# Kernel tuning notes

Measured on AMD Instinct MI355X. Metric: run time of the kernel, lower is better.

The kernel has to match this reference:

```python
import jax, jax.numpy as jnp
import numpy as np
from jax import lax


def setup_inputs() -> dict:
    key = jax.random.key(0)
    ks = jax.random.split(key, 10)
    T, S, B, L, H = 256, 1024, 1, 2, 1024
    sc = 1.0 / np.sqrt(H)  # torch LSTM/Linear init scale
    return {
        "input_sequence": jax.random.normal(ks[0], (T, B, H), jnp.float32),
        "encoder_out": jax.random.normal(ks[1], (S, B, H), jnp.float32),
        "hidden_state": jax.random.normal(ks[2], (L, B, H), jnp.float32),
        "cell_state": jax.random.normal(ks[3], (L, B, H), jnp.float32),
        "w_ih": jax.random.uniform(ks[4], (L, 4 * H, H), jnp.float32, -sc, sc),
        "w_hh": jax.random.uniform(ks[5], (L, 4 * H, H), jnp.float32, -sc, sc),
        "b_ih": jax.random.uniform(ks[6], (L, 4 * H), jnp.float32, -sc, sc),
        "b_hh": jax.random.uniform(ks[7], (L, 4 * H), jnp.float32, -sc, sc),
        "w_concat": jax.random.uniform(ks[8], (H, 2 * H), jnp.float32, -sc, sc),
        "b_concat": jax.random.uniform(ks[9], (H,), jnp.float32, -sc, sc),
    }


def reference(input_sequence, encoder_out, hidden_state, cell_state,
              w_ih, w_hh, b_ih, b_hh, w_concat, b_concat):
    T = input_sequence.shape[0]
    L = w_ih.shape[0]

    def step(carry, _):
        h, c, x = carry  # h,c: [L,1,H]; x: [1,H]
        hs, cs = [], []
        inp = x
        for l in range(L):  # stacked LSTM layers (small, static)
            gates = inp @ w_ih[l].T + h[l] @ w_hh[l].T + b_ih[l] + b_hh[l]  # [1,4H]
            i, f, g, o = jnp.split(gates, 4, axis=-1)  # torch gate order i,f,g,o
            c_new = jax.nn.sigmoid(f) * c[l] + jax.nn.sigmoid(i) * jnp.tanh(g)
            h_new = jax.nn.sigmoid(o) * jnp.tanh(c_new)
            hs.append(h_new)
            cs.append(c_new)
            inp = h_new
        h = jnp.stack(hs)  # [L,1,H]
        c = jnp.stack(cs)
        # Luong 'dot' attention: scores [S,1,1] = encoder_out @ h_last^T (B=1)
        scores = jnp.einsum('sbh,bh->sb', encoder_out, h[-1])[..., None]
        w = jax.nn.softmax(scores, axis=0)               # softmax over source dim
        context = jnp.sum(encoder_out * w, axis=0)        # [1,H]
        cat = jnp.concatenate([context, h[-1]], axis=-1)  # [1,2H]
        attn_h = jnp.tanh(cat @ w_concat.T + b_concat)    # [1,H]
        return (h, c, attn_h), attn_h

    init = (hidden_state, cell_state, hidden_state[-1])
    _, outputs = lax.scan(step, init, None, length=T)
    return outputs  # [T,1,H]
```

## Files before the change

kernel.cpp:

```cpp
#include <hip/hip_runtime.h>
#include <cstdint>
#include <cstddef>


#define TSTEPS 256
#define HDIM   1024
#define NBLK   256
#define NTHR   256

#define WS_X    0
#define WS_H0   1024
#define WS_H1   3072
#define WS_C0   5120
#define WS_C1   6144
#define WS_SC   7168
#define WS_Y2   8192
#define WS_MT   16384
#define SLOTS_OFF_BYTES ((size_t)(WS_MT + 1024 * 1024) * sizeof(float))
#define SLOT_STRIDE 16

__device__ __forceinline__ float wred_sum(float v) {
#pragma unroll
  for (int m = 32; m >= 1; m >>= 1) v += __shfl_xor(v, m, 64);
  return v;
}
__device__ __forceinline__ float wred_max(float v) {
#pragma unroll
  for (int m = 32; m >= 1; m >>= 1) v = fmaxf(v, __shfl_xor(v, m, 64));
  return v;
}

__device__ __forceinline__ float2 aload2(const float* p) {
  unsigned long long u = __hip_atomic_load((unsigned long long*)(uintptr_t)p,
                                           __ATOMIC_RELAXED, __HIP_MEMORY_SCOPE_AGENT);
  float2 r;
  r.x = __uint_as_float((unsigned)u);
  r.y = __uint_as_float((unsigned)(u >> 32));
  return r;
}
__device__ __forceinline__ void astoref(float* p, float v) {
  __hip_atomic_store((unsigned*)p, __float_as_uint(v), __ATOMIC_RELAXED,
                     __HIP_MEMORY_SCOPE_AGENT);
}

__device__ __forceinline__ void gbar(int* slots, int gen) {
  __syncthreads();
  if (threadIdx.x == 0)
    __hip_atomic_store(&slots[blockIdx.x * SLOT_STRIDE], gen, __ATOMIC_RELAXED,
                       __HIP_MEMORY_SCOPE_AGENT);
  int ok;
  do {
    int v = __hip_atomic_load(&slots[threadIdx.x * SLOT_STRIDE], __ATOMIC_RELAXED,
                              __HIP_MEMORY_SCOPE_AGENT);
    ok = (v >= gen);
    if (!ok) __builtin_amdgcn_s_sleep(2);
  } while (!__syncthreads_and(ok));
}

__device__ __forceinline__ float sigmoidf_(float x) { return 1.f / (1.f + __expf(-x)); }

__device__ __forceinline__ void load16_plain(const float* base, int l, float* r) {
#pragma unroll
  for (int i = 0; i < 8; ++i) {
    float2 a = *(const float2*)(base + 2 * l + 128 * i);
    r[2 * i] = a.x; r[2 * i + 1] = a.y;
  }
}
__device__ __forceinline__ void load16_agent(const float* base, int l, float* r) {
#pragma unroll
  for (int i = 0; i < 8; ++i) {
    float2 a = aload2(base + 2 * l + 128 * i);
    r[2 * i] = a.x; r[2 * i + 1] = a.y;
  }
}
__device__ __forceinline__ float dotrow(const float* row, int l, const float* x) {
  float p = 0.f;
#pragma unroll
  for (int i = 0; i < 8; ++i) {
    float2 wv = *(const float2*)(row + 2 * l + 128 * i);
    p += wv.x * x[2 * i] + wv.y * x[2 * i + 1];
  }
  return p;
}

__device__ __forceinline__ void lstm_cell(
    int k, int l, const float* __restrict__ wih, const float* __restrict__ whh,
    const float* __restrict__ bih, const float* __restrict__ bhh,
    const float* xr, const float* hr, const float* cold_src, float* cdst,
    float* hdst) {
  float gs[4];
#pragma unroll
  for (int g = 0; g < 4; ++g) {
    const float* wi = wih + (size_t)(g * HDIM + k) * HDIM;
    const float* wh = whh + (size_t)(g * HDIM + k) * HDIM;
    float p = dotrow(wi, l, xr) + dotrow(wh, l, hr);
    gs[g] = wred_sum(p);
  }
  if (l == 0) {
    float ig = sigmoidf_(gs[0] + bih[k] + bhh[k]);
    float fg = sigmoidf_(gs[1] + bih[HDIM + k] + bhh[HDIM + k]);
    float gg = tanhf(gs[2] + bih[2 * HDIM + k] + bhh[2 * HDIM + k]);
    float og = sigmoidf_(gs[3] + bih[3 * HDIM + k] + bhh[3 * HDIM + k]);
    float cn = fg * cold_src[k] + ig * gg;
    cdst[k] = cn;
    astoref(hdst + k, og * tanhf(cn));
  }
}

__global__ void __launch_bounds__(NTHR) decoder_persist(
    const float* __restrict__ enc,
    const float* __restrict__ hid,
    const float* __restrict__ cell,
    const float* __restrict__ w_ih,
    const float* __restrict__ w_hh,
    const float* __restrict__ b_ih,
    const float* __restrict__ b_hh,
    const float* __restrict__ wcat,
    const float* __restrict__ bcat,
    float* __restrict__ out,
    float* __restrict__ ws) {
  const int b = blockIdx.x;
  const int tid = threadIdx.x;
  const int w = tid >> 6;
  const int l = tid & 63;
  int* slots = (int*)((char*)ws + SLOTS_OFF_BYTES);
  float* MT = ws + WS_MT;

  {
    const int j0 = b << 2;
    const float* wr0 = wcat + (size_t)(j0 + 0) * 2048;
    const float* wr1 = wcat + (size_t)(j0 + 1) * 2048;
    const float* wr2 = wcat + (size_t)(j0 + 2) * 2048;
    const float* wr3 = wcat + (size_t)(j0 + 3) * 2048;
#pragma unroll
    for (int ii = 0; ii < 4; ++ii) {
      int s = (w << 8) + (ii << 6) + l;
      const float* er = enc + (size_t)s * HDIM;
      float a0 = 0.f, a1 = 0.f, a2 = 0.f, a3 = 0.f;
      for (int hh = 0; hh < HDIM; hh += 4) {
        float4 ev = *(const float4*)(er + hh);
        float4 w0 = *(const float4*)(wr0 + hh);
        float4 w1 = *(const float4*)(wr1 + hh);
        float4 w2 = *(const float4*)(wr2 + hh);
        float4 w3 = *(const float4*)(wr3 + hh);
        a0 += ev.x * w0.x + ev.y * w0.y + ev.z * w0.z + ev.w * w0.w;
        a1 += ev.x * w1.x + ev.y * w1.y + ev.z * w1.z + ev.w * w1.w;
        a2 += ev.x * w2.x + ev.y * w2.y + ev.z * w2.z + ev.w * w2.w;
        a3 += ev.x * w3.x + ev.y * w3.y + ev.z * w3.z + ev.w * w3.w;
      }
      MT[(size_t)(j0 + 0) * HDIM + s] = a0;
      MT[(size_t)(j0 + 1) * HDIM + s] = a1;
      MT[(size_t)(j0 + 2) * HDIM + s] = a2;
      MT[(size_t)(j0 + 3) * HDIM + s] = a3;
    }
  }
  __syncthreads();

  const float* wih1 = w_ih + (size_t)4096 * 1024;
  const float* whh1 = w_hh + (size_t)4096 * 1024;
  const float* bih1 = b_ih + 4096;
  const float* bhh1 = b_hh + 4096;

  for (int t = 0; t < TSTEPS; ++t) {
    const int par = t & 1;
    float* h0r = ws + WS_H0 + par * 1024;
    float* h0w = ws + WS_H0 + (par ^ 1) * 1024;
    float* h1r = ws + WS_H1 + par * 1024;
    float* h1w = ws + WS_H1 + (par ^ 1) * 1024;

    {
      const int k = (b << 2) + w;
      float xr[16], hr[16];
      if (t == 0) {
        load16_plain(hid + HDIM, l, xr);
        load16_plain(hid, l, hr);
      } else {
        load16_agent(ws + WS_X, l, xr);
        load16_agent(h0r, l, hr);
      }
      const float* csrc = (t == 0) ? cell : (ws + WS_C0);
      lstm_cell(k, l, w_ih, w_hh, b_ih, b_hh, xr, hr, csrc, ws + WS_C0, h0w);
    }
    gbar(slots, t * 4 + 1);

    {
      const int k = (b << 2) + w;
      float xr[16], hr[16];
      load16_agent(h0w, l, xr);
      if (t == 0) load16_plain(hid + HDIM, l, hr);
      else        load16_agent(h1r, l, hr);
      const float* csrc = (t == 0) ? (cell + HDIM) : (ws + WS_C1);
      lstm_cell(k, l, wih1, whh1, bih1, bhh1, xr, hr, csrc, ws + WS_C1, h1w);
    }
    gbar(slots, t * 4 + 2);

    {
      float hv[16];
      load16_agent(h1w, l, hv);
#pragma unroll
      for (int rr = 0; rr < 2; ++rr) {
        int r = (b << 2) + ((w & 1) << 1) + rr;
        const float* row = (w < 2) ? (enc + (size_t)r * HDIM)
                                   : (wcat + (size_t)r * 2048 + HDIM);
        float p = dotrow(row, l, hv);
        p = wred_sum(p);
        if (l == 0) {
          if (w < 2) astoref(ws + WS_SC + r, p);
          else       ws[WS_Y2 + r] = p;
        }
      }
    }
    gbar(slots, t * 4 + 3);

    {
      const int j = (b << 2) + w;
      float sc[16];
      load16_agent(ws + WS_SC, l, sc);
      float m = sc[0];
#pragma unroll
      for (int i = 1; i < 16; ++i) m = fmaxf(m, sc[i]);
      m = wred_max(m);
      float e[16];
      float d = 0.f;
#pragma unroll
      for (int i = 0; i < 16; ++i) { e[i] = __expf(sc[i] - m); d += e[i]; }
      d = wred_sum(d);
      const float* mrow = MT + (size_t)j * HDIM;
      float p = 0.f;
#pragma unroll
      for (int i = 0; i < 8; ++i) {
        float2 mv = *(const float2*)(mrow + 2 * l + 128 * i);
        p += mv.x * e[2 * i] + mv.y * e[2 * i + 1];
      }
      p = wred_sum(p);
      if (l == 0) {
        float a = tanhf(p / d + ws[WS_Y2 + j] + bcat[j]);
        astoref(ws + WS_X + j, a);
        out[(size_t)t * HDIM + j] = a;
      }
    }
    gbar(slots, t * 4 + 4);
  }
}

extern "C" void kernel_launch(void* const* d_in, const int* in_sizes, int n_in,
                              void* d_out, int out_size, void* d_ws, size_t ws_size,
                              hipStream_t stream) {
  const float* enc  = (const float*)d_in[1];
  const float* hid  = (const float*)d_in[2];
  const float* cel  = (const float*)d_in[3];
  const float* wih  = (const float*)d_in[4];
  const float* whh  = (const float*)d_in[5];
  const float* bih  = (const float*)d_in[6];
  const float* bhh  = (const float*)d_in[7];
  const float* wcat = (const float*)d_in[8];
  const float* bcat = (const float*)d_in[9];
  float* out = (float*)d_out;
  float* ws  = (float*)d_ws;

  hipLaunchKernelGGL(decoder_persist, dim3(NBLK), dim3(NTHR), 0, stream,
                     enc, hid, cel, wih, whh, bih, bhh, wcat, bcat, out, ws);
}
```

Baseline: 4.104 ms.

## Widen blocks to 1024 threads and stage shared vectors in LDS

Raises threads per block from 256 to 1024, with each wave now computing one gate row per hidden unit, or a half row or chunk in the later phases, instead of four gate rows per wave. The shared x/h vectors are loaded once per block into LDS rather than per wave through atomic float2 loads. Partial sums are combined through shared memory, and the softmax is spread across all 1024 threads. This shortens the serial per-wave work between grid barriers, at the cost of extra __syncthreads and a heavier barrier with more threads per block. It also caches the w_concat rows in LDS for the precompute.

```diff
diff --git a/kernel.cpp b/kernel.cpp
--- a/kernel.cpp
+++ b/kernel.cpp
@@ -6,7 +6,7 @@
 #define TSTEPS 256
 #define HDIM   1024
 #define NBLK   256
-#define NTHR   256
+#define NTHR   1024
 
 #define WS_X    0
 #define WS_H0   1024
@@ -14,7 +14,6 @@
 #define WS_C0   5120
 #define WS_C1   6144
 #define WS_SC   7168
-#define WS_Y2   8192
 #define WS_MT   16384
 #define SLOTS_OFF_BYTES ((size_t)(WS_MT + 1024 * 1024) * sizeof(float))
 #define SLOT_STRIDE 16
@@ -30,13 +29,10 @@
   return v;
 }
 
-__device__ __forceinline__ float2 aload2(const float* p) {
-  unsigned long long u = __hip_atomic_load((unsigned long long*)(uintptr_t)p,
-                                           __ATOMIC_RELAXED, __HIP_MEMORY_SCOPE_AGENT);
-  float2 r;
-  r.x = __uint_as_float((unsigned)u);
-  r.y = __uint_as_float((unsigned)(u >> 32));
-  return r;
+__device__ __forceinline__ float aloadf(const float* p) {
+  unsigned u = __hip_atomic_load((const unsigned*)(uintptr_t)p,
+                                 __ATOMIC_RELAXED, __HIP_MEMORY_SCOPE_AGENT);
+  return __uint_as_float(u);
 }
 __device__ __forceinline__ void astoref(float* p, float v) {
   __hip_atomic_store((unsigned*)p, __float_as_uint(v), __ATOMIC_RELAXED,
@@ -48,66 +44,20 @@
   if (threadIdx.x == 0)
     __hip_atomic_store(&slots[blockIdx.x * SLOT_STRIDE], gen, __ATOMIC_RELAXED,
                        __HIP_MEMORY_SCOPE_AGENT);
-  int ok;
+  int ok = 1;
   do {
-    int v = __hip_atomic_load(&slots[threadIdx.x * SLOT_STRIDE], __ATOMIC_RELAXED,
-                              __HIP_MEMORY_SCOPE_AGENT);
-    ok = (v >= gen);
-    if (!ok) __builtin_amdgcn_s_sleep(2);
+    if (threadIdx.x < NBLK) {
+      int v = __hip_atomic_load(&slots[threadIdx.x * SLOT_STRIDE],
+                                __ATOMIC_RELAXED, __HIP_MEMORY_SCOPE_AGENT);
+      ok = (v >= gen);
+      if (!ok) __builtin_amdgcn_s_sleep(2);
+    }
   } while (!__syncthreads_and(ok));
 }
 
 __device__ __forceinline__ float sigmoidf_(float x) { return 1.f / (1.f + __expf(-x)); }
 
-__device__ __forceinline__ void load16_plain(const float* base, int l, float* r) {
-#pragma unroll
-  for (int i = 0; i < 8; ++i) {
-    float2 a = *(const float2*)(base + 2 * l + 128 * i);
-    r[2 * i] = a.x; r[2 * i + 1] = a.y;
-  }
-}
-__device__ __forceinline__ void load16_agent(const float* base, int l, float* r) {
-#pragma unroll
-  for (int i = 0; i < 8; ++i) {
-    float2 a = aload2(base + 2 * l + 128 * i);
-    r[2 * i] = a.x; r[2 * i + 1] = a.y;
-  }
-}
-__device__ __forceinline__ float dotrow(const float* row, int l, const float* x) {
-  float p = 0.f;
-#pragma unroll
-  for (int i = 0; i < 8; ++i) {
-    float2 wv = *(const float2*)(row + 2 * l + 128 * i);
-    p += wv.x * x[2 * i] + wv.y * x[2 * i + 1];
-  }
-  return p;
-}
-
-__device__ __forceinline__ void lstm_cell(
-    int k, int l, const float* __restrict__ wih, const float* __restrict__ whh,
-    const float* __restrict__ bih, const float* __restrict__ bhh,
-    const float* xr, const float* hr, const float* cold_src, float* cdst,
-    float* hdst) {
-  float gs[4];
-#pragma unroll
-  for (int g = 0; g < 4; ++g) {
-    const float* wi = wih + (size_t)(g * HDIM + k) * HDIM;
-    const float* wh = whh + (size_t)(g * HDIM + k) * HDIM;
-    float p = dotrow(wi, l, xr) + dotrow(wh, l, hr);
-    gs[g] = wred_sum(p);
-  }
-  if (l == 0) {
-    float ig = sigmoidf_(gs[0] + bih[k] + bhh[k]);
-    float fg = sigmoidf_(gs[1] + bih[HDIM + k] + bhh[HDIM + k]);
-    float gg = tanhf(gs[2] + bih[2 * HDIM + k] + bhh[2 * HDIM + k]);
-    float og = sigmoidf_(gs[3] + bih[3 * HDIM + k] + bhh[3 * HDIM + k]);
-    float cn = fg * cold_src[k] + ig * gg;
-    cdst[k] = cn;
-    astoref(hdst + k, og * tanhf(cn));
-  }
-}
-
-__global__ void __launch_bounds__(NTHR) decoder_persist(
+__global__ void __launch_bounds__(NTHR, 4) decoder_persist(
     const float* __restrict__ enc,
     const float* __restrict__ hid,
     const float* __restrict__ cell,
@@ -125,34 +75,41 @@
   const int l = tid & 63;
   int* slots = (int*)((char*)ws + SLOTS_OFF_BYTES);
   float* MT = ws + WS_MT;
+  const int j0 = b << 2;
+
+  __shared__ float sh_x[HDIM];
+  __shared__ float sh_h[HDIM];
+  __shared__ __align__(16) float sh_es[HDIM];
+  __shared__ __align__(16) float sh_wc[4][HDIM];
+  __shared__ float sh_g[16];
+  __shared__ float sh_r[16];
+  __shared__ float sh_p[16];
+  __shared__ float sh_q[16];
+  __shared__ float sh_y2[4];
 
   {
-    const int j0 = b << 2;
-    const float* wr0 = wcat + (size_t)(j0 + 0) * 2048;
-    const float* wr1 = wcat + (size_t)(j0 + 1) * 2048;
-    const float* wr2 = wcat + (size_t)(j0 + 2) * 2048;
-    const float* wr3 = wcat + (size_t)(j0 + 3) * 2048;
-#pragma unroll
-    for (int ii = 0; ii < 4; ++ii) {
-      int s = (w << 8) + (ii << 6) + l;
-      const float* er = enc + (size_t)s * HDIM;
-      float a0 = 0.f, a1 = 0.f, a2 = 0.f, a3 = 0.f;
-      for (int hh = 0; hh < HDIM; hh += 4) {
-        float4 ev = *(const float4*)(er + hh);
-        float4 w0 = *(const float4*)(wr0 + hh);
-        float4 w1 = *(const float4*)(wr1 + hh);
-        float4 w2 = *(const float4*)(wr2 + hh);
-        float4 w3 = *(const float4*)(wr3 + hh);
-        a0 += ev.x * w0.x + ev.y * w0.y + ev.z * w0.z + ev.w * w0.w;
-        a1 += ev.x * w1.x + ev.y * w1.y + ev.z * w1.z + ev.w * w1.w;
-        a2 += ev.x * w2.x + ev.y * w2.y + ev.z * w2.z + ev.w * w2.w;
-        a3 += ev.x * w3.x + ev.y * w3.y + ev.z * w3.z + ev.w * w3.w;
-      }
-      MT[(size_t)(j0 + 0) * HDIM + s] = a0;
-      MT[(size_t)(j0 + 1) * HDIM + s] = a1;
-      MT[(size_t)(j0 + 2) * HDIM + s] = a2;
-      MT[(size_t)(j0 + 3) * HDIM + s] = a3;
-    }
+#pragma unroll
+    for (int rep = 0; rep < 4; ++rep)
+      sh_wc[rep][tid & 1023] = wcat[(size_t)(j0 + rep) * 2048 + tid];
+    __syncthreads();
+    const int s = (w << 6) + l;
+    const float* er = enc + (size_t)s * HDIM;
+    float a0 = 0.f, a1 = 0.f, a2 = 0.f, a3 = 0.f;
+    for (int hh = 0; hh < HDIM; hh += 4) {
+      float4 ev = *(const float4*)(er + hh);
+      float4 w0 = *(const float4*)&sh_wc[0][hh];
+      float4 w1 = *(const float4*)&sh_wc[1][hh];
+      float4 w2 = *(const float4*)&sh_wc[2][hh];
+      float4 w3 = *(const float4*)&sh_wc[3][hh];
+      a0 += ev.x * w0.x + ev.y * w0.y + ev.z * w0.z + ev.w * w0.w;
+      a1 += ev.x * w1.x + ev.y * w1.y + ev.z * w1.z + ev.w * w1.w;
+      a2 += ev.x * w2.x + ev.y * w2.y + ev.z * w2.z + ev.w * w2.w;
+      a3 += ev.x * w3.x + ev.y * w3.y + ev.z * w3.z + ev.w * w3.w;
+    }
+    MT[(size_t)(j0 + 0) * HDIM + s] = a0;
+    MT[(size_t)(j0 + 1) * HDIM + s] = a1;
+    MT[(size_t)(j0 + 2) * HDIM + s] = a2;
+    MT[(size_t)(j0 + 3) * HDIM + s] = a3;
   }
   __syncthreads();
 
@@ -169,74 +126,137 @@
     float* h1w = ws + WS_H1 + (par ^ 1) * 1024;
 
     {
-      const int k = (b << 2) + w;
-      float xr[16], hr[16];
       if (t == 0) {
-        load16_plain(hid + HDIM, l, xr);
-        load16_plain(hid, l, hr);
+        sh_x[tid] = hid[HDIM + tid];
+        sh_h[tid] = hid[tid];
       } else {
-        load16_agent(ws + WS_X, l, xr);
-        load16_agent(h0r, l, hr);
-      }
-      const float* csrc = (t == 0) ? cell : (ws + WS_C0);
-      lstm_cell(k, l, w_ih, w_hh, b_ih, b_hh, xr, hr, csrc, ws + WS_C0, h0w);
+        sh_x[tid] = aloadf(ws + WS_X + tid);
+        sh_h[tid] = aloadf(h0r + tid);
+      }
+      __syncthreads();
+      const int d = w >> 2, g = w & 3, k = j0 + d;
+      const float* wi = w_ih + (size_t)((g << 10) + k) * HDIM;
+      const float* wh = w_hh + (size_t)((g << 10) + k) * HDIM;
+      float p = 0.f;
+#pragma unroll
+      for (int i = 0; i < 8; ++i) {
+        float2 wv = *(const float2*)(wi + 2 * l + 128 * i);
+        float2 hv = *(const float2*)(wh + 2 * l + 128 * i);
+        float2 xv = *(const float2*)(sh_x + 2 * l + 128 * i);
+        float2 rv = *(const float2*)(sh_h + 2 * l + 128 * i);
+        p += wv.x * xv.x + wv.y * xv.y + hv.x * rv.x + hv.y * rv.y;
+      }
+      p = wred_sum(p);
+      if (l == 0) sh_g[w] = p;
+      __syncthreads();
+      if (tid < 4) {
+        const int k2 = j0 + tid;
+        float ig = sigmoidf_(sh_g[(tid << 2) + 0] + b_ih[k2] + b_hh[k2]);
+        float fg = sigmoidf_(sh_g[(tid << 2) + 1] + b_ih[HDIM + k2] + b_hh[HDIM + k2]);
+        float gg = tanhf   (sh_g[(tid << 2) + 2] + b_ih[2 * HDIM + k2] + b_hh[2 * HDIM + k2]);
+        float og = sigmoidf_(sh_g[(tid << 2) + 3] + b_ih[3 * HDIM + k2] + b_hh[3 * HDIM + k2]);
+        float cold = (t == 0) ? cell[k2] : ws[WS_C0 + k2];
+        float cn = fg * cold + ig * gg;
+        ws[WS_C0 + k2] = cn;
+        astoref(h0w + k2, og * tanhf(cn));
+      }
     }
     gbar(slots, t * 4 + 1);
 
     {
-      const int k = (b << 2) + w;
-      float xr[16], hr[16];
-      load16_agent(h0w, l, xr);
-      if (t == 0) load16_plain(hid + HDIM, l, hr);
-      else        load16_agent(h1r, l, hr);
-      const float* csrc = (t == 0) ? (cell + HDIM) : (ws + WS_C1);
-      lstm_cell(k, l, wih1, whh1, bih1, bhh1, xr, hr, csrc, ws + WS_C1, h1w);
+      sh_x[tid] = aloadf(h0w + tid);
+      if (t == 0) sh_h[tid] = hid[HDIM + tid];
+      else        sh_h[tid] = aloadf(h1r + tid);
+      __syncthreads();
+      const int d = w >> 2, g = w & 3, k = j0 + d;
+      const float* wi = wih1 + (size_t)((g << 10) + k) * HDIM;
+      const float* wh = whh1 + (size_t)((g << 10) + k) * HDIM;
+      float p = 0.f;
+#pragma unroll
+      for (int i = 0; i < 8; ++i) {
+        float2 wv = *(const float2*)(wi + 2 * l + 128 * i);
+        float2 hv = *(const float2*)(wh + 2 * l + 128 * i);
+        float2 xv = *(const float2*)(sh_x + 2 * l + 128 * i);
+        float2 rv = *(const float2*)(sh_h + 2 * l + 128 * i);
+        p += wv.x * xv.x + wv.y * xv.y + hv.x * rv.x + hv.y * rv.y;
+      }
+      p = wred_sum(p);
+      if (l == 0) sh_g[w] = p;
+      __syncthreads();
+      if (tid < 4) {
+        const int k2 = j0 + tid;
+        float ig = sigmoidf_(sh_g[(tid << 2) + 0] + bih1[k2] + bhh1[k2]);
+        float fg = sigmoidf_(sh_g[(tid << 2) + 1] + bih1[HDIM + k2] + bhh1[HDIM + k2]);
+        float gg = tanhf   (sh_g[(tid << 2) + 2] + bih1[2 * HDIM + k2] + bhh1[2 * HDIM + k2]);
+        float og = sigmoidf_(sh_g[(tid << 2) + 3] + bih1[3 * HDIM + k2] + bhh1[3 * HDIM + k2]);
+        float cold = (t == 0) ? cell[HDIM + k2] : ws[WS_C1 + k2];
+        float cn = fg * cold + ig * gg;
+        ws[WS_C1 + k2] = cn;
+        astoref(h1w + k2, og * tanhf(cn));
+      }
     }
     gbar(slots, t * 4 + 2);
 
     {
-      float hv[16];
-      load16_agent(h1w, l, hv);
-#pragma unroll
-      for (int rr = 0; rr < 2; ++rr) {
-        int r = (b << 2) + ((w & 1) << 1) + rr;
-        const float* row = (w < 2) ? (enc + (size_t)r * HDIM)
-                                   : (wcat + (size_t)r * 2048 + HDIM);
-        float p = dotrow(row, l, hv);
-        p = wred_sum(p);
-        if (l == 0) {
-          if (w < 2) astoref(ws + WS_SC + r, p);
-          else       ws[WS_Y2 + r] = p;
+      sh_x[tid] = aloadf(h1w + tid);
+      __syncthreads();
+      const int rw = w & 7;
+      const int d = rw >> 1, half = rw & 1;
+      const float* row = (w < 8)
+          ? (enc  + (size_t)(j0 + d) * 1024 + half * 512)
+          : (wcat + (size_t)(j0 + d) * 2048 + 1024 + half * 512);
+      float p = 0.f;
+#pragma unroll
+      for (int i = 0; i < 4; ++i) {
+        float2 wv = *(const float2*)(row + 2 * l + 128 * i);
+        float2 xv = *(const float2*)(sh_x + half * 512 + 2 * l + 128 * i);
+        p += wv.x * xv.x + wv.y * xv.y;
+      }
+      p = wred_sum(p);
+      if (l == 0) sh_g[w] = p;
+      __syncthreads();
+      if (tid < 8) {
+        if (tid < 4) {
+          float sc = sh_g[2 * tid] + sh_g[2 * tid + 1];
+          astoref(ws + WS_SC + j0 + tid, sc);
+        } else {
+          int d2 = tid - 4;
+          sh_y2[d2] = sh_g[8 + 2 * d2] + sh_g[9 + 2 * d2];
         }
       }
     }
     gbar(slots, t * 4 + 3);
 
     {
-      const int j = (b << 2) + w;
-      float sc[16];
-      load16_agent(ws + WS_SC, l, sc);
-      float m = sc[0];
-#pragma unroll
-      for (int i = 1; i < 16; ++i) m = fmaxf(m, sc[i]);
-      m = wred_max(m);
-      float e[16];
-      float d = 0.f;
-#pragma unroll
-      for (int i = 0; i < 16; ++i) { e[i] = __expf(sc[i] - m); d += e[i]; }
-      d = wred_sum(d);
-      const float* mrow = MT + (size_t)j * HDIM;
-      float p = 0.f;
-#pragma unroll
-      for (int i = 0; i < 8; ++i) {
-        float2 mv = *(const float2*)(mrow + 2 * l + 128 * i);
-        p += mv.x * e[2 * i] + mv.y * e[2 * i + 1];
-      }
-      p = wred_sum(p);
-      if (l == 0) {
-        float a = tanhf(p / d + ws[WS_Y2 + j] + bcat[j]);
-        astoref(ws + WS_X + j, a);
-        out[(size_t)t * HDIM + j] = a;
+      float sc = aloadf(ws + WS_SC + tid);
+      float m = wred_max(sc);
+      if (l == 0) sh_r[w] = m;
+      __syncthreads();
+      float bm = sh_r[0];
+#pragma unroll
+      for (int i = 1; i < 16; ++i) bm = fmaxf(bm, sh_r[i]);
+      float e = __expf(sc - bm);
+      sh_es[tid] = e;
+      float ps = wred_sum(e);
+      if (l == 0) sh_p[w] = ps;
+      __syncthreads();
+      const int d = w & 3, chunk = w >> 2, k = j0 + d;
+      const float* mrow = MT + (size_t)k * HDIM + (chunk << 8);
+      float4 mv = *(const float4*)(mrow + 4 * l);
+      float4 ev = *(const float4*)(&sh_es[(chunk << 8) + 4 * l]);
+      float p = mv.x * ev.x + mv.y * ev.y + mv.z * ev.z + mv.w * ev.w;
+      p = wred_sum(p);
+      if (l == 0) sh_q[w] = p;
+      __syncthreads();
+      if (tid < 4) {
+        const int k2 = j0 + tid;
+        float denom = 0.f;
+#pragma unroll
+        for (int i = 0; i < 16; ++i) denom += sh_p[i];
+        float numer = sh_q[tid] + sh_q[4 + tid] + sh_q[8 + tid] + sh_q[12 + tid];
+        float a = tanhf(numer / denom + sh_y2[tid] + bcat[k2]);
+        astoref(ws + WS_X + k2, a);
+        out[(size_t)t * HDIM + k2] = a;
       }
     }
     gbar(slots, t * 4 + 4);
```

Measured after the change: 4.685 ms. +14.2%, slower.

## Replace grid barriers with tagged dataflow slots and register-resident weights

Applied to the files above, without the earlier changes.

Removes the four grid-wide barriers per timestep. Producers now write 64-bit values that carry a generation tag, and consumer waves poll for them per element, then stage the data into LDS under workgroup-scope flags. Block size doubles to 512 threads so each block's LSTM weight rows, attention rows and the precomputed M rows stay in registers for the whole run instead of being reloaded every step. Correctness depends on the tags matching, and spin-waiting inside LDS could deadlock if waves are not scheduled fairly. Register pressure is much higher.

```diff
diff --git a/kernel.cpp b/kernel.cpp
--- a/kernel.cpp
+++ b/kernel.cpp
@@ -6,18 +6,15 @@
 #define TSTEPS 256
 #define HDIM   1024
 #define NBLK   256
-#define NTHR   256
-
-#define WS_X    0
-#define WS_H0   1024
-#define WS_H1   3072
-#define WS_C0   5120
-#define WS_C1   6144
-#define WS_SC   7168
-#define WS_Y2   8192
-#define WS_MT   16384
-#define SLOTS_OFF_BYTES ((size_t)(WS_MT + 1024 * 1024) * sizeof(float))
-#define SLOT_STRIDE 16
+#define NTHR   512
+
+typedef unsigned long long u64;
+
+#define WX   0
+#define WH0  1024
+#define WH1  3072
+#define WSC  5120
+#define WMT  6144
 
 __device__ __forceinline__ float wred_sum(float v) {
 #pragma unroll
@@ -29,85 +26,48 @@
   for (int m = 32; m >= 1; m >>= 1) v = fmaxf(v, __shfl_xor(v, m, 64));
   return v;
 }
-
-__device__ __forceinline__ float2 aload2(const float* p) {
-  unsigned long long u = __hip_atomic_load((unsigned long long*)(uintptr_t)p,
-                                           __ATOMIC_RELAXED, __HIP_MEMORY_SCOPE_AGENT);
-  float2 r;
-  r.x = __uint_as_float((unsigned)u);
-  r.y = __uint_as_float((unsigned)(u >> 32));
-  return r;
-}
-__device__ __forceinline__ void astoref(float* p, float v) {
-  __hip_atomic_store((unsigned*)p, __float_as_uint(v), __ATOMIC_RELAXED,
-                     __HIP_MEMORY_SCOPE_AGENT);
-}
-
-__device__ __forceinline__ void gbar(int* slots, int gen) {
-  __syncthreads();
-  if (threadIdx.x == 0)
-    __hip_atomic_store(&slots[blockIdx.x * SLOT_STRIDE], gen, __ATOMIC_RELAXED,
-                       __HIP_MEMORY_SCOPE_AGENT);
-  int ok;
-  do {
-    int v = __hip_atomic_load(&slots[threadIdx.x * SLOT_STRIDE], __ATOMIC_RELAXED,
-                              __HIP_MEMORY_SCOPE_AGENT);
-    ok = (v >= gen);
-    if (!ok) __builtin_amdgcn_s_sleep(2);
-  } while (!__syncthreads_and(ok));
-}
-
-__device__ __forceinline__ float sigmoidf_(float x) { return 1.f / (1.f + __expf(-x)); }
-
-__device__ __forceinline__ void load16_plain(const float* base, int l, float* r) {
-#pragma unroll
-  for (int i = 0; i < 8; ++i) {
-    float2 a = *(const float2*)(base + 2 * l + 128 * i);
-    r[2 * i] = a.x; r[2 * i + 1] = a.y;
-  }
-}
-__device__ __forceinline__ void load16_agent(const float* base, int l, float* r) {
-#pragma unroll
-  for (int i = 0; i < 8; ++i) {
-    float2 a = aload2(base + 2 * l + 128 * i);
-    r[2 * i] = a.x; r[2 * i + 1] = a.y;
-  }
-}
-__device__ __forceinline__ float dotrow(const float* row, int l, const float* x) {
-  float p = 0.f;
-#pragma unroll
-  for (int i = 0; i < 8; ++i) {
-    float2 wv = *(const float2*)(row + 2 * l + 128 * i);
-    p += wv.x * x[2 * i] + wv.y * x[2 * i + 1];
-  }
-  return p;
-}
-
-__device__ __forceinline__ void lstm_cell(
-    int k, int l, const float* __restrict__ wih, const float* __restrict__ whh,
-    const float* __restrict__ bih, const float* __restrict__ bhh,
-    const float* xr, const float* hr, const float* cold_src, float* cdst,
-    float* hdst) {
-  float gs[4];
-#pragma unroll
-  for (int g = 0; g < 4; ++g) {
-    const float* wi = wih + (size_t)(g * HDIM + k) * HDIM;
-    const float* wh = whh + (size_t)(g * HDIM + k) * HDIM;
-    float p = dotrow(wi, l, xr) + dotrow(wh, l, hr);
-    gs[g] = wred_sum(p);
-  }
-  if (l == 0) {
-    float ig = sigmoidf_(gs[0] + bih[k] + bhh[k]);
-    float fg = sigmoidf_(gs[1] + bih[HDIM + k] + bhh[HDIM + k]);
-    float gg = tanhf(gs[2] + bih[2 * HDIM + k] + bhh[2 * HDIM + k]);
-    float og = sigmoidf_(gs[3] + bih[3 * HDIM + k] + bhh[3 * HDIM + k]);
-    float cn = fg * cold_src[k] + ig * gg;
-    cdst[k] = cn;
-    astoref(hdst + k, og * tanhf(cn));
-  }
-}
-
-__global__ void __launch_bounds__(NTHR) decoder_persist(
+__device__ __forceinline__ void astore64(u64* p, int tag, float v) {
+  u64 x = ((u64)(unsigned)tag << 32) | (u64)(unsigned)__float_as_uint(v);
+  __hip_atomic_store(p, x, __ATOMIC_RELAXED, __HIP_MEMORY_SCOPE_AGENT);
+}
+__device__ __forceinline__ u64 aload64(const u64* p) {
+  return __hip_atomic_load(p, __ATOMIC_RELAXED, __HIP_MEMORY_SCOPE_AGENT);
+}
+__device__ __forceinline__ void lds_set(int* f, int v) {
+  __hip_atomic_store(f, v, __ATOMIC_RELEASE, __HIP_MEMORY_SCOPE_WORKGROUP);
+}
+__device__ __forceinline__ void lds_wait(int* f, int v) {
+  while (__hip_atomic_load(f, __ATOMIC_ACQUIRE, __HIP_MEMORY_SCOPE_WORKGROUP) < v) {}
+}
+__device__ __forceinline__ float sigf(float x) { return 1.f / (1.f + __expf(-x)); }
+
+__device__ __forceinline__ void stage_poll(const u64* slots, int tag, float* buf,
+                                           int* flag, int fval, int l) {
+  float v[16];
+  unsigned miss = 0xffffu;
+  while (miss) {
+#pragma unroll
+    for (int i = 0; i < 16; ++i) {
+      if (miss & (1u << i)) {
+        u64 x = aload64(slots + l + 64 * i);
+        if ((int)(x >> 32) == tag) { v[i] = __uint_as_float((unsigned)x); miss &= ~(1u << i); }
+      }
+    }
+    if (miss == 0xffffu) __builtin_amdgcn_s_sleep(8);
+    else if (miss)       __builtin_amdgcn_s_sleep(1);
+  }
+#pragma unroll
+  for (int i = 0; i < 16; ++i) buf[l + 64 * i] = v[i];
+  lds_set(flag, fval);
+}
+__device__ __forceinline__ void stage_direct(const float* src, float* buf,
+                                             int* flag, int fval, int l) {
+#pragma unroll
+  for (int i = 0; i < 16; ++i) buf[l + 64 * i] = src[l + 64 * i];
+  lds_set(flag, fval);
+}
+
+__global__ void __launch_bounds__(NTHR, 1) decoder_persist(
     const float* __restrict__ enc,
     const float* __restrict__ hid,
     const float* __restrict__ cell,
@@ -118,128 +78,200 @@
     const float* __restrict__ wcat,
     const float* __restrict__ bcat,
     float* __restrict__ out,
-    float* __restrict__ ws) {
-  const int b = blockIdx.x;
-  const int tid = threadIdx.x;
-  const int w = tid >> 6;
-  const int l = tid & 63;
-  int* slots = (int*)((char*)ws + SLOTS_OFF_BYTES);
-  float* MT = ws + WS_MT;
+    float* __restrict__ ws_f) {
+  u64* W = (u64*)ws_f;
+  float* MTp = (float*)(W + WMT);
+  const int b = blockIdx.x, tid = threadIdx.x;
+  const int w = tid >> 6, l = tid & 63;
+  const int j0 = b << 2;
+  const int d = w >> 1, gp = w & 1;
+  const int k = j0 + d;
+
+  __shared__ __align__(16) float bxA[HDIM], bhA[HDIM], bxB[HDIM], bhB[HDIM],
+                                 bhC[HDIM], bsD[HDIM];
+  __shared__ int fxA, fhA, fxB, fhB, fhC, fsD;
+  __shared__ float pG[4], pO[4];
+  __shared__ int pF[4];
+  if (tid == 0) { fxA = fhA = fxB = fhB = fhC = fsD = 0; }
+  if (tid < 4) pF[tid] = 0;
+
+  const int ga = gp * 2;
+  const float* WI0 = w_ih;
+  const float* WH0p = w_hh;
+  const float* WI1 = w_ih + (size_t)4096 * 1024;
+  const float* WH1p = w_hh + (size_t)4096 * 1024;
+  float wiA0[16], wiA1[16], whA0[16], whA1[16];
+  float wiB0[16], wiB1[16], whB0[16], whB1[16];
+#pragma unroll
+  for (int i = 0; i < 16; ++i) {
+    int col = l + 64 * i;
+    wiA0[i] = WI0[(size_t)((ga    ) * 1024 + k) * 1024 + col];
+    wiA1[i] = WI0[(size_t)((ga + 1) * 1024 + k) * 1024 + col];
+    whA0[i] = WH0p[(size_t)((ga    ) * 1024 + k) * 1024 + col];
+    whA1[i] = WH0p[(size_t)((ga + 1) * 1024 + k) * 1024 + col];
+    wiB0[i] = WI1[(size_t)((ga    ) * 1024 + k) * 1024 + col];
+    wiB1[i] = WI1[(size_t)((ga + 1) * 1024 + k) * 1024 + col];
+    whB0[i] = WH1p[(size_t)((ga    ) * 1024 + k) * 1024 + col];
+    whB1[i] = WH1p[(size_t)((ga + 1) * 1024 + k) * 1024 + col];
+  }
+  const int cd = (w < 4) ? w : (w - 4);
+  const float* crp = (w < 4) ? (enc + (size_t)(j0 + cd) * 1024)
+                             : (wcat + (size_t)(j0 + cd) * 2048 + 1024);
+  float crow[16];
+#pragma unroll
+  for (int i = 0; i < 16; ++i) crow[i] = crp[l + 64 * i];
+  float bA[4], bB[4];
+#pragma unroll
+  for (int g = 0; g < 4; ++g) {
+    bA[g] = b_ih[g * 1024 + k] + b_hh[g * 1024 + k];
+    bB[g] = b_ih[4096 + g * 1024 + k] + b_hh[4096 + g * 1024 + k];
+  }
+  float c0 = cell[k], c1 = cell[1024 + k];
+  float bc = bcat[j0 + cd];
 
   {
-    const int j0 = b << 2;
-    const float* wr0 = wcat + (size_t)(j0 + 0) * 2048;
-    const float* wr1 = wcat + (size_t)(j0 + 1) * 2048;
-    const float* wr2 = wcat + (size_t)(j0 + 2) * 2048;
-    const float* wr3 = wcat + (size_t)(j0 + 3) * 2048;
-#pragma unroll
-    for (int ii = 0; ii < 4; ++ii) {
-      int s = (w << 8) + (ii << 6) + l;
-      const float* er = enc + (size_t)s * HDIM;
+#pragma unroll
+    for (int r = 0; r < 4; ++r) {
+      float* wcb = (r == 0) ? bxA : (r == 1) ? bhA : (r == 2) ? bxB : bhB;
+      for (int idx = tid; idx < HDIM; idx += NTHR)
+        wcb[idx] = wcat[(size_t)(j0 + r) * 2048 + idx];
+    }
+    __syncthreads();
+#pragma unroll
+    for (int rep = 0; rep < 2; ++rep) {
+      int s = (w << 6) + l + (rep << 9);
+      const float* er = enc + (size_t)s * 1024;
       float a0 = 0.f, a1 = 0.f, a2 = 0.f, a3 = 0.f;
-      for (int hh = 0; hh < HDIM; hh += 4) {
+      for (int hh = 0; hh < 1024; hh += 4) {
         float4 ev = *(const float4*)(er + hh);
-        float4 w0 = *(const float4*)(wr0 + hh);
-        float4 w1 = *(const float4*)(wr1 + hh);
-        float4 w2 = *(const float4*)(wr2 + hh);
-        float4 w3 = *(const float4*)(wr3 + hh);
-        a0 += ev.x * w0.x + ev.y * w0.y + ev.z * w0.z + ev.w * w0.w;
-        a1 += ev.x * w1.x + ev.y * w1.y + ev.z * w1.z + ev.w * w1.w;
-        a2 += ev.x * w2.x + ev.y * w2.y + ev.z * w2.z + ev.w * w2.w;
-        a3 += ev.x * w3.x + ev.y * w3.y + ev.z * w3.z + ev.w * w3.w;
-      }
-      MT[(size_t)(j0 + 0) * HDIM + s] = a0;
-      MT[(size_t)(j0 + 1) * HDIM + s] = a1;
-      MT[(size_t)(j0 + 2) * HDIM + s] = a2;
-      MT[(size_t)(j0 + 3) * HDIM + s] = a3;
-    }
+        float4 q0 = *(const float4*)(bxA + hh);
+        float4 q1 = *(const float4*)(bhA + hh);
+        float4 q2 = *(const float4*)(bxB + hh);
+        float4 q3 = *(const float4*)(bhB + hh);
+        a0 += ev.x * q0.x + ev.y * q0.y + ev.z * q0.z + ev.w * q0.w;
+        a1 += ev.x * q1.x + ev.y * q1.y + ev.z * q1.z + ev.w * q1.w;
+        a2 += ev.x * q2.x + ev.y * q2.y + ev.z * q2.z + ev.w * q2.w;
+        a3 += ev.x * q3.x + ev.y * q3.y + ev.z * q3.z + ev.w * q3.w;
+      }
+      MTp[(size_t)(j0 + 0) * 1024 + s] = a0;
+      MTp[(size_t)(j0 + 1) * 1024 + s] = a1;
+      MTp[(size_t)(j0 + 2) * 1024 + s] = a2;
+      MTp[(size_t)(j0 + 3) * 1024 + s] = a3;
+    }
+    __syncthreads();
+  }
+  float mt[16];
+  if (w >= 4) {
+#pragma unroll
+    for (int i = 0; i < 16; ++i)
+      mt[i] = MTp[(size_t)(j0 + w - 4) * 1024 + l + 64 * i];
   }
   __syncthreads();
 
-  const float* wih1 = w_ih + (size_t)4096 * 1024;
-  const float* whh1 = w_hh + (size_t)4096 * 1024;
-  const float* bih1 = b_ih + 4096;
-  const float* bhh1 = b_hh + 4096;
-
+  float y2 = 0.f;
   for (int t = 0; t < TSTEPS; ++t) {
     const int par = t & 1;
-    float* h0r = ws + WS_H0 + par * 1024;
-    float* h0w = ws + WS_H0 + (par ^ 1) * 1024;
-    float* h1r = ws + WS_H1 + par * 1024;
-    float* h1w = ws + WS_H1 + (par ^ 1) * 1024;
-
+    const int gen = t + 1;
+
+    if (w == 6) {
+      if (t == 0) stage_direct(hid + HDIM, bxA, &fxA, gen, l);
+      else        stage_poll(W + WX, t, bxA, &fxA, gen, l);
+    }
+    if (w == 7) {
+      if (t == 0) stage_direct(hid, bhA, &fhA, gen, l);
+      else        stage_poll(W + WH0 + (par ^ 1) * 1024, t, bhA, &fhA, gen, l);
+    }
+    lds_wait(&fxA, gen);
+    lds_wait(&fhA, gen);
     {
-      const int k = (b << 2) + w;
-      float xr[16], hr[16];
-      if (t == 0) {
-        load16_plain(hid + HDIM, l, xr);
-        load16_plain(hid, l, hr);
+      float a0 = 0.f, a1 = 0.f;
+#pragma unroll
+      for (int i = 0; i < 16; ++i) {
+        float xv = bxA[l + 64 * i], hv = bhA[l + 64 * i];
+        a0 += wiA0[i] * xv + whA0[i] * hv;
+        a1 += wiA1[i] * xv + whA1[i] * hv;
+      }
+      a0 = wred_sum(a0);
+      a1 = wred_sum(a1);
+      if (gp == 1) {
+        if (l == 0) { pG[d] = a0; pO[d] = a1; lds_set(&pF[d], 2 * t + 1); }
+      } else if (l == 0) {
+        lds_wait(&pF[d], 2 * t + 1);
+        float gi = sigf(a0 + bA[0]), gf = sigf(a1 + bA[1]);
+        float gg = tanhf(pG[d] + bA[2]), go = sigf(pO[d] + bA[3]);
+        c0 = gf * c0 + gi * gg;
+        astore64(W + WH0 + par * 1024 + k, gen, go * tanhf(c0));
+      }
+    }
+
+    if (w == 6) stage_poll(W + WH0 + par * 1024, gen, bxB, &fxB, gen, l);
+    if (w == 7) {
+      if (t == 0) stage_direct(hid + HDIM, bhB, &fhB, gen, l);
+      else        stage_poll(W + WH1 + (par ^ 1) * 1024, t, bhB, &fhB, gen, l);
+    }
+    lds_wait(&fxB, gen);
+    lds_wait(&fhB, gen);
+    {
+      float a0 = 0.f, a1 = 0.f;
+#pragma unroll
+      for (int i = 0; i < 16; ++i) {
+        float xv = bxB[l + 64 * i], hv = bhB[l + 64 * i];
+        a0 += wiB0[i] * xv + whB0[i] * hv;
+        a1 += wiB1[i] * xv + whB1[i] * hv;
+      }
+      a0 = wred_sum(a0);
+      a1 = wred_sum(a1);
+      if (gp == 1) {
+        if (l == 0) { pG[d] = a0; pO[d] = a1; lds_set(&pF[d], 2 * t + 2); }
+      } else if (l == 0) {
+        lds_wait(&pF[d], 2 * t + 2);
+        float gi = sigf(a0 + bB[0]), gf = sigf(a1 + bB[1]);
+        float gg = tanhf(pG[d] + bB[2]), go = sigf(pO[d] + bB[3]);
+        c1 = gf * c1 + gi * gg;
+        astore64(W + WH1 + par * 1024 + k, gen, go * tanhf(c1));
+      }
+    }
+
+    if (w == 6) stage_poll(W + WH1 + par * 1024, gen, bhC, &fhC, gen, l);
+    lds_wait(&fhC, gen);
+    {
+      float p = 0.f;
+#pragma unroll
+      for (int i = 0; i < 16; ++i) p += crow[i] * bhC[l + 64 * i];
+      p = wred_sum(p);
+      if (w < 4) {
+        if (l == 0) astore64(W + WSC + j0 + w, gen, p);
       } else {
-        load16_agent(ws + WS_X, l, xr);
-        load16_agent(h0r, l, hr);
-      }
-      const float* csrc = (t == 0) ? cell : (ws + WS_C0);
-      lstm_cell(k, l, w_ih, w_hh, b_ih, b_hh, xr, hr, csrc, ws + WS_C0, h0w);
-    }
-    gbar(slots, t * 4 + 1);
-
-    {
-      const int k = (b << 2) + w;
-      float xr[16], hr[16];
-      load16_agent(h0w, l, xr);
-      if (t == 0) load16_plain(hid + HDIM, l, hr);
-      else        load16_agent(h1r, l, hr);
-      const float* csrc = (t == 0) ? (cell + HDIM) : (ws + WS_C1);
-      lstm_cell(k, l, wih1, whh1, bih1, bhh1, xr, hr, csrc, ws + WS_C1, h1w);
-    }
-    gbar(slots, t * 4 + 2);
-
-    {
-      float hv[16];
-      load16_agent(h1w, l, hv);
-#pragma unroll
-      for (int rr = 0; rr < 2; ++rr) {
-        int r = (b << 2) + ((w & 1) << 1) + rr;
-        const float* row = (w < 2) ? (enc + (size_t)r * HDIM)
-                                   : (wcat + (size_t)r * 2048 + HDIM);
-        float p = dotrow(row, l, hv);
-        p = wred_sum(p);
-        if (l == 0) {
-          if (w < 2) astoref(ws + WS_SC + r, p);
-          else       ws[WS_Y2 + r] = p;
-        }
-      }
-    }
-    gbar(slots, t * 4 + 3);
-
-    {
-      const int j = (b << 2) + w;
-      float sc[16];
-      load16_agent(ws + WS_SC, l, sc);
-      float m = sc[0];
-#pragma unroll
-      for (int i = 1; i < 16; ++i) m = fmaxf(m, sc[i]);
-      m = wred_max(m);
-      float e[16];
-      float d = 0.f;
-#pragma unroll
-      for (int i = 0; i < 16; ++i) { e[i] = __expf(sc[i] - m); d += e[i]; }
-      d = wred_sum(d);
-      const float* mrow = MT + (size_t)j * HDIM;
-      float p = 0.f;
-#pragma unroll
-      for (int i = 0; i < 8; ++i) {
-        float2 mv = *(const float2*)(mrow + 2 * l + 128 * i);
-        p += mv.x * e[2 * i] + mv.y * e[2 * i + 1];
-      }
-      p = wred_sum(p);
+        y2 = p;
+      }
+    }
+
+    if (w == 7) stage_poll(W + WSC, gen, bsD, &fsD, gen, l);
+    if (w >= 4) {
+      lds_wait(&fsD, gen);
+      float sv[16];
+#pragma unroll
+      for (int i = 0; i < 16; ++i) sv[i] = bsD[l + 64 * i];
+      float mx = sv[0];
+#pragma unroll
+      for (int i = 1; i < 16; ++i) mx = fmaxf(mx, sv[i]);
+      mx = wred_max(mx);
+      float den = 0.f, num = 0.f;
+#pragma unroll
+      for (int i = 0; i < 16; ++i) {
+        float e = __expf(sv[i] - mx);
+        den += e;
+        num += e * mt[i];
+      }
+      den = wred_sum(den);
+      num = wred_sum(num);
       if (l == 0) {
-        float a = tanhf(p / d + ws[WS_Y2 + j] + bcat[j]);
-        astoref(ws + WS_X + j, a);
-        out[(size_t)t * HDIM + j] = a;
-      }
-    }
-    gbar(slots, t * 4 + 4);
+        int j = j0 + (w - 4);
+        float val = tanhf(num / den + y2 + bc);
+        astore64(W + WX + j, gen, val);
+        out[(size_t)t * HDIM + j] = val;
+      }
+    }
   }
 }
 
```

Result: slower. 7.769 ms (+89.3%).
